# Optimization experiments

Hardware: AMD Instinct MI355X
Metric: run time of the kernel (lower is better)

Reference implementation:

```python
import jax, jax.numpy as jnp
import numpy as np

EPS = 1e-5
ALPHA = 32.0


def setup_inputs() -> dict:
    key = jax.random.key(0)
    k1, k2 = jax.random.split(key)
    M, D, K = 131072, 256, 512
    x = jax.random.normal(k1, (M, D), dtype=jnp.float32)
    ln_weight = jnp.ones((D,), dtype=jnp.float32)
    ln_bias = jnp.zeros((D,), dtype=jnp.float32)
    cluster_center = jax.random.uniform(k2, (K, D), dtype=jnp.float32)
    return {"x": x, "ln_weight": ln_weight, "ln_bias": ln_bias,
            "cluster_center": cluster_center}


def reference(x, ln_weight, ln_bias, cluster_center):
    # CustomLayerNorm: (x - mean) / (std + eps) * w + b  (std unbiased=False,
    # NOTE eps is added to std, not variance, matching the torch module)
    mean = x.mean(axis=-1, keepdims=True)
    std = jnp.sqrt(((x - mean) ** 2).mean(axis=-1, keepdims=True))
    xn = (x - mean) / (std + EPS) * ln_weight + ln_bias

    # Euclidean cdist via sum-of-squares + GEMM, then sqrt (as in source)
    x_sq = (xn * xn).sum(axis=-1, keepdims=True)            # (M, 1)
    c_sq = (cluster_center * cluster_center).sum(axis=-1)   # (K,)
    d2 = x_sq + c_sq[None, :] - 2.0 * (xn @ cluster_center.T)
    x_distance = jnp.sqrt(d2)                               # (M, K)

    # NegSoftAssign: exp(-alpha * d / mean_d), normalized over last dim
    d_mean = x_distance.mean(axis=-1, keepdims=True)
    logits = -ALPHA * (x_distance / d_mean)
    x_distance_assign = jax.nn.softmax(logits, axis=-1)     # (M, K)

    x_rec = x_distance_assign @ cluster_center              # (M, D)
    return (x_distance, x_distance_assign, x_rec)
```

## Files before the change

kernel.cpp:

```cpp
#include <hip/hip_runtime.h>
#include <hip/hip_bf16.h>
#include <cstdint>

#define M_ROWS 131072
#define D_DIM  256
#define K_CL   512

typedef __attribute__((ext_vector_type(4))) float  f4;
typedef __attribute__((ext_vector_type(8))) short  bfrag;
typedef __attribute__((ext_vector_type(4))) float  ffrag;

#define MFMA16(A,B,C) __builtin_amdgcn_mfma_f32_16x16x32_bf16((A),(B),(C),0,0,0)

__device__ __forceinline__ unsigned short f2bf(float f) {
    unsigned int u = __float_as_uint(f);
    u += 0x7FFFu + ((u >> 16) & 1u);
    return (unsigned short)(u >> 16);
}
__device__ __forceinline__ float bf2f(unsigned short u) {
    return __uint_as_float(((unsigned int)u) << 16);
}

__global__ void prep_kernel(const float* __restrict__ C,
                            unsigned short* __restrict__ Cb,
                            unsigned short* __restrict__ Ct,
                            float* __restrict__ csq)
{
    __shared__ unsigned short lds[64 * 264];
    const int tid = threadIdx.x;
    const int kb  = blockIdx.x * 64;
    const int r   = tid >> 2;
    const int q   = tid & 3;

    const float* cr = C + (size_t)(kb + r) * D_DIM;
    float s = 0.f;
    #pragma unroll
    for (int i = 0; i < 16; ++i) {
        const int j = q * 16 + i;
        f4 v = *(const f4*)(cr + j * 4);
        unsigned short u0 = f2bf(v[0]), u1 = f2bf(v[1]), u2 = f2bf(v[2]), u3 = f2bf(v[3]);
        *(ushort4*)(Cb + (size_t)(kb + r) * D_DIM + j * 4) = make_ushort4(u0, u1, u2, u3);
        *(ushort4*)(lds + r * 264 + j * 4)                  = make_ushort4(u0, u1, u2, u3);
        float f0 = bf2f(u0), f1 = bf2f(u1), f2_ = bf2f(u2), f3 = bf2f(u3);
        s += f0 * f0 + f1 * f1 + f2_ * f2_ + f3 * f3;
    }
    s += __shfl_xor(s, 1, 64);
    s += __shfl_xor(s, 2, 64);
    if (q == 0) csq[kb + r] = s;
    __syncthreads();

    #pragma unroll
    for (int c = 0; c < 16; ++c) {
        ushort4 p = make_ushort4(lds[(c * 4 + 0) * 264 + tid],
                                 lds[(c * 4 + 1) * 264 + tid],
                                 lds[(c * 4 + 2) * 264 + tid],
                                 lds[(c * 4 + 3) * 264 + tid]);
        *(ushort4*)(Ct + (size_t)tid * K_CL + kb + c * 4) = p;
    }
}

__global__ __launch_bounds__(256)
void fused_kernel(const float* __restrict__ x,
                  const float* __restrict__ lnw,
                  const float* __restrict__ lnb,
                  const unsigned short* __restrict__ Cb,
                  const unsigned short* __restrict__ Ct,
                  const float* __restrict__ csq,
                  float* __restrict__ out0,
                  float* __restrict__ out1,
                  float* __restrict__ out2)
{
    __shared__ __align__(16) char smem[51712];
    unsigned short* xn_s = (unsigned short*)smem;
    unsigned short* as_s = (unsigned short*)(smem + 16896);
    float* csq_s = (float*)(smem + 16896);
    float* red_a = (float*)(smem + 50176);
    float* red_b = (float*)(smem + 50688);
    float* xsq_s = (float*)(smem + 51200);
    float* sc_s  = (float*)(smem + 51328);
    float* mn_s  = (float*)(smem + 51456);
    float* rn_s  = (float*)(smem + 51584);

    const int tid = threadIdx.x;
    const int w   = tid >> 6;
    const int l   = tid & 63;
    const int g   = l >> 4;
    const int cl  = l & 15;
    const int m0  = blockIdx.x * 32;

    csq_s[tid]       = csq[tid];
    csq_s[tid + 256] = csq[tid + 256];

    {
        const int row = tid >> 3, sub = tid & 7;
        const float* xr = x + (size_t)(m0 + row) * D_DIM;
        f4 xv[8];
        float sum = 0.f, ss = 0.f;
        #pragma unroll
        for (int i = 0; i < 8; ++i) {
            xv[i] = *(const f4*)(xr + (i * 8 + sub) * 4);
            #pragma unroll
            for (int c = 0; c < 4; ++c) { float v = xv[i][c]; sum += v; ss += v * v; }
        }
        #pragma unroll
        for (int msk = 1; msk < 8; msk <<= 1) {
            sum += __shfl_xor(sum, msk, 64);
            ss  += __shfl_xor(ss,  msk, 64);
        }
        const float mean = sum * (1.0f / 256.0f);
        float var = ss * (1.0f / 256.0f) - mean * mean;
        var = fmaxf(var, 0.0f);
        const float inv = 1.0f / (sqrtf(var) + 1e-5f);

        float xsq = 0.f;
        #pragma unroll
        for (int i = 0; i < 8; ++i) {
            f4 wv = *(const f4*)(lnw + (i * 8 + sub) * 4);
            f4 bv = *(const f4*)(lnb + (i * 8 + sub) * 4);
            unsigned short u0, u1, u2, u3;
            {
                float a0 = (xv[i][0] - mean) * inv * wv[0] + bv[0];
                float a1 = (xv[i][1] - mean) * inv * wv[1] + bv[1];
                float a2 = (xv[i][2] - mean) * inv * wv[2] + bv[2];
                float a3 = (xv[i][3] - mean) * inv * wv[3] + bv[3];
                u0 = f2bf(a0); u1 = f2bf(a1); u2 = f2bf(a2); u3 = f2bf(a3);
                float b0 = bf2f(u0), b1 = bf2f(u1), b2 = bf2f(u2), b3 = bf2f(u3);
                xsq += b0 * b0 + b1 * b1 + b2 * b2 + b3 * b3;
            }
            *(ushort4*)(xn_s + row * 264 + (i * 8 + sub) * 4) = make_ushort4(u0, u1, u2, u3);
        }
        #pragma unroll
        for (int msk = 1; msk < 8; msk <<= 1) xsq += __shfl_xor(xsq, msk, 64);
        if (sub == 0) xsq_s[row] = xsq;
    }
    __syncthreads();

    const int nb = w * 128;
    ffrag acc[2][8];
    #pragma unroll
    for (int rt = 0; rt < 2; ++rt)
        #pragma unroll
        for (int nt = 0; nt < 8; ++nt)
            acc[rt][nt] = (ffrag){0.f, 0.f, 0.f, 0.f};
    {
        bfrag a[2][8];
        #pragma unroll
        for (int rt = 0; rt < 2; ++rt)
            #pragma unroll
            for (int ks = 0; ks < 8; ++ks)
                a[rt][ks] = *(const bfrag*)(xn_s + (rt * 16 + cl) * 264 + ks * 32 + g * 8);
        #pragma unroll
        for (int nt = 0; nt < 8; ++nt) {
            const unsigned short* bp = Cb + (size_t)(nb + nt * 16 + cl) * D_DIM + g * 8;
            #pragma unroll
            for (int ks = 0; ks < 8; ++ks) {
                bfrag b = *(const bfrag*)(bp + ks * 32);
                acc[0][nt] = MFMA16(a[0][ks], b, acc[0][nt]);
                acc[1][nt] = MFMA16(a[1][ks], b, acc[1][nt]);
            }
        }
    }

    float xsq_r[2][4];
    #pragma unroll
    for (int rt = 0; rt < 2; ++rt)
        #pragma unroll
        for (int r = 0; r < 4; ++r)
            xsq_r[rt][r] = xsq_s[rt * 16 + g * 4 + r];

    #pragma unroll
    for (int nt = 0; nt < 8; ++nt) {
        const float cs = csq_s[nb + nt * 16 + cl];
        #pragma unroll
        for (int rt = 0; rt < 2; ++rt)
            #pragma unroll
            for (int r = 0; r < 4; ++r) {
                float d2 = xsq_r[rt][r] + cs - 2.0f * acc[rt][nt][r];
                float d  = sqrtf(fmaxf(d2, 0.0f));
                acc[rt][nt][r] = d;
                out0[(size_t)(m0 + rt * 16 + g * 4 + r) * K_CL + nb + nt * 16 + cl] = d;
            }
    }

    {
        float s[2][4], mn[2][4];
        #pragma unroll
        for (int rt = 0; rt < 2; ++rt)
            #pragma unroll
            for (int r = 0; r < 4; ++r) { s[rt][r] = acc[rt][0][r]; mn[rt][r] = acc[rt][0][r]; }
        #pragma unroll
        for (int nt = 1; nt < 8; ++nt)
            #pragma unroll
            for (int rt = 0; rt < 2; ++rt)
                #pragma unroll
                for (int r = 0; r < 4; ++r) {
                    s[rt][r]  += acc[rt][nt][r];
                    mn[rt][r]  = fminf(mn[rt][r], acc[rt][nt][r]);
                }
        #pragma unroll
        for (int msk = 1; msk < 16; msk <<= 1)
            #pragma unroll
            for (int rt = 0; rt < 2; ++rt)
                #pragma unroll
                for (int r = 0; r < 4; ++r) {
                    s[rt][r]  += __shfl_xor(s[rt][r],  msk, 64);
                    mn[rt][r]  = fminf(mn[rt][r], __shfl_xor(mn[rt][r], msk, 64));
                }
        if (cl == 0) {
            #pragma unroll
            for (int rt = 0; rt < 2; ++rt)
                #pragma unroll
                for (int r = 0; r < 4; ++r) {
                    red_a[w * 32 + rt * 16 + g * 4 + r] = s[rt][r];
                    red_b[w * 32 + rt * 16 + g * 4 + r] = mn[rt][r];
                }
        }
    }
    __syncthreads();
    if (tid < 32) {
        float t0 = red_a[tid] + red_a[32 + tid] + red_a[64 + tid] + red_a[96 + tid];
        float mv = fminf(fminf(red_b[tid], red_b[32 + tid]),
                         fminf(red_b[64 + tid], red_b[96 + tid]));
        sc_s[tid] = 16384.0f / t0;
        mn_s[tid] = mv;
    }
    __syncthreads();

    {
        float sc_r[2][4], mnr[2][4], es[2][4];
        #pragma unroll
        for (int rt = 0; rt < 2; ++rt)
            #pragma unroll
            for (int r = 0; r < 4; ++r) {
                sc_r[rt][r] = sc_s[rt * 16 + g * 4 + r];
                mnr[rt][r]  = mn_s[rt * 16 + g * 4 + r];
                es[rt][r]   = 0.f;
            }
        #pragma unroll
        for (int nt = 0; nt < 8; ++nt)
            #pragma unroll
            for (int rt = 0; rt < 2; ++rt)
                #pragma unroll
                for (int r = 0; r < 4; ++r) {
                    float p = __expf((mnr[rt][r] - acc[rt][nt][r]) * sc_r[rt][r]);
                    acc[rt][nt][r] = p;
                    es[rt][r] += p;
                }
        #pragma unroll
        for (int msk = 1; msk < 16; msk <<= 1)
            #pragma unroll
            for (int rt = 0; rt < 2; ++rt)
                #pragma unroll
                for (int r = 0; r < 4; ++r)
                    es[rt][r] += __shfl_xor(es[rt][r], msk, 64);
        if (cl == 0) {
            #pragma unroll
            for (int rt = 0; rt < 2; ++rt)
                #pragma unroll
                for (int r = 0; r < 4; ++r)
                    red_a[w * 32 + rt * 16 + g * 4 + r] = es[rt][r];
        }
    }
    __syncthreads();
    if (tid < 32)
        rn_s[tid] = 1.0f / (red_a[tid] + red_a[32 + tid] + red_a[64 + tid] + red_a[96 + tid]);
    __syncthreads();

    {
        float rn_r[2][4];
        #pragma unroll
        for (int rt = 0; rt < 2; ++rt)
            #pragma unroll
            for (int r = 0; r < 4; ++r)
                rn_r[rt][r] = rn_s[rt * 16 + g * 4 + r];
        #pragma unroll
        for (int nt = 0; nt < 8; ++nt)
            #pragma unroll
            for (int rt = 0; rt < 2; ++rt)
                #pragma unroll
                for (int r = 0; r < 4; ++r) {
                    float av = acc[rt][nt][r] * rn_r[rt][r];
                    out1[(size_t)(m0 + rt * 16 + g * 4 + r) * K_CL + nb + nt * 16 + cl] = av;
                    as_s[(rt * 16 + g * 4 + r) * 520 + nb + nt * 16 + cl] = f2bf(av);
                }
    }
    __syncthreads();

    {
        ffrag acc2[2][4];
        #pragma unroll
        for (int rt = 0; rt < 2; ++rt)
            #pragma unroll
            for (int nt = 0; nt < 4; ++nt)
                acc2[rt][nt] = (ffrag){0.f, 0.f, 0.f, 0.f};
        const int db = w * 64;
        #pragma unroll
        for (int kt = 0; kt < 16; ++kt) {
            bfrag a0 = *(const bfrag*)(as_s + (cl)      * 520 + kt * 32 + g * 8);
            bfrag a1 = *(const bfrag*)(as_s + (16 + cl) * 520 + kt * 32 + g * 8);
            #pragma unroll
            for (int nt = 0; nt < 4; ++nt) {
                bfrag b = *(const bfrag*)(Ct + (size_t)(db + nt * 16 + cl) * K_CL + kt * 32 + g * 8);
                acc2[0][nt] = MFMA16(a0, b, acc2[0][nt]);
                acc2[1][nt] = MFMA16(a1, b, acc2[1][nt]);
            }
        }
        #pragma unroll
        for (int rt = 0; rt < 2; ++rt)
            #pragma unroll
            for (int nt = 0; nt < 4; ++nt)
                #pragma unroll
                for (int r = 0; r < 4; ++r)
                    out2[(size_t)(m0 + rt * 16 + g * 4 + r) * D_DIM + db + nt * 16 + cl]
                        = acc2[rt][nt][r];
    }
}

extern "C" void kernel_launch(void* const* d_in, const int* in_sizes, int n_in,
                              void* d_out, int out_size, void* d_ws, size_t ws_size,
                              hipStream_t stream)
{
    const float* x   = (const float*)d_in[0];
    const float* lnw = (const float*)d_in[1];
    const float* lnb = (const float*)d_in[2];
    const float* C   = (const float*)d_in[3];

    float* out0 = (float*)d_out;
    float* out1 = out0 + (size_t)M_ROWS * K_CL;
    float* out2 = out1 + (size_t)M_ROWS * K_CL;

    unsigned short* Cb = (unsigned short*)d_ws;
    unsigned short* Ct = Cb + (size_t)K_CL * D_DIM;
    float*          cs = (float*)((char*)d_ws + 2u * K_CL * D_DIM * 2u);

    prep_kernel<<<8, 256, 0, stream>>>(C, Cb, Ct, cs);
    fused_kernel<<<M_ROWS / 32, 256, 0, stream>>>(x, lnw, lnb, Cb, Ct, cs,
                                                  out0, out1, out2);
}
```

Before: 330.8 us.

## Halve rows per block to 16 and alias LDS buffers for higher occupancy

Each block now processes 16 rows instead of 32, so each wave holds one 16-row MFMA tile and about half as many accumulator registers. The LDS layout is shrunk by aliasing the assignment buffer onto the normalized-x buffer. Launch bounds now request 4 blocks per CU. The intent is to raise occupancy and hide memory latency. In exchange, every cluster-center B fragment loaded from global memory now feeds half as many MFMAs, which doubles B traffic per row, and twice as many blocks are launched.

Result: slower. 544.7 us (+64.7%).

```diff
diff --git a/kernel.cpp b/kernel.cpp
--- a/kernel.cpp
+++ b/kernel.cpp
@@ -5,6 +5,7 @@
 #define M_ROWS 131072
 #define D_DIM  256
 #define K_CL   512
+#define ROWS_B 16
 
 typedef __attribute__((ext_vector_type(4))) float  f4;
 typedef __attribute__((ext_vector_type(8))) short  bfrag;
@@ -59,7 +60,7 @@
     }
 }
 
-__global__ __launch_bounds__(256)
+__global__ __launch_bounds__(256, 4)
 void fused_kernel(const float* __restrict__ x,
                   const float* __restrict__ lnw,
                   const float* __restrict__ lnb,
@@ -70,40 +71,41 @@
                   float* __restrict__ out1,
                   float* __restrict__ out2)
 {
-    __shared__ __align__(16) char smem[51712];
+    __shared__ __align__(16) char smem[19456];
     unsigned short* xn_s = (unsigned short*)smem;
-    unsigned short* as_s = (unsigned short*)(smem + 16896);
-    float* csq_s = (float*)(smem + 16896);
-    float* red_a = (float*)(smem + 50176);
-    float* red_b = (float*)(smem + 50688);
-    float* xsq_s = (float*)(smem + 51200);
-    float* sc_s  = (float*)(smem + 51328);
-    float* mn_s  = (float*)(smem + 51456);
-    float* rn_s  = (float*)(smem + 51584);
+    unsigned short* as_s = (unsigned short*)smem;
+    float* csq_s = (float*)(smem + 16640);
+    float* red_a = (float*)(smem + 18688);
+    float* red_b = (float*)(smem + 18944);
+    float* xsq_s = (float*)(smem + 19200);
+    float* sc_s  = (float*)(smem + 19264);
+    float* mn_s  = (float*)(smem + 19328);
+    float* rn_s  = (float*)(smem + 19392);
 
     const int tid = threadIdx.x;
     const int w   = tid >> 6;
     const int l   = tid & 63;
     const int g   = l >> 4;
     const int cl  = l & 15;
-    const int m0  = blockIdx.x * 32;
+    const int m0  = blockIdx.x * ROWS_B;
+    const int row = g * 4;
 
     csq_s[tid]       = csq[tid];
     csq_s[tid + 256] = csq[tid + 256];
 
     {
-        const int row = tid >> 3, sub = tid & 7;
-        const float* xr = x + (size_t)(m0 + row) * D_DIM;
-        f4 xv[8];
+        const int rr  = tid >> 4, sub = tid & 15;
+        const float* xr = x + (size_t)(m0 + rr) * D_DIM;
+        f4 xv[4];
         float sum = 0.f, ss = 0.f;
         #pragma unroll
-        for (int i = 0; i < 8; ++i) {
-            xv[i] = *(const f4*)(xr + (i * 8 + sub) * 4);
+        for (int i = 0; i < 4; ++i) {
+            xv[i] = *(const f4*)(xr + (i * 16 + sub) * 4);
             #pragma unroll
             for (int c = 0; c < 4; ++c) { float v = xv[i][c]; sum += v; ss += v * v; }
         }
         #pragma unroll
-        for (int msk = 1; msk < 8; msk <<= 1) {
+        for (int msk = 1; msk < 16; msk <<= 1) {
             sum += __shfl_xor(sum, msk, 64);
             ss  += __shfl_xor(ss,  msk, 64);
         }
@@ -114,205 +116,162 @@
 
         float xsq = 0.f;
         #pragma unroll
-        for (int i = 0; i < 8; ++i) {
-            f4 wv = *(const f4*)(lnw + (i * 8 + sub) * 4);
-            f4 bv = *(const f4*)(lnb + (i * 8 + sub) * 4);
-            unsigned short u0, u1, u2, u3;
-            {
-                float a0 = (xv[i][0] - mean) * inv * wv[0] + bv[0];
-                float a1 = (xv[i][1] - mean) * inv * wv[1] + bv[1];
-                float a2 = (xv[i][2] - mean) * inv * wv[2] + bv[2];
-                float a3 = (xv[i][3] - mean) * inv * wv[3] + bv[3];
-                u0 = f2bf(a0); u1 = f2bf(a1); u2 = f2bf(a2); u3 = f2bf(a3);
-                float b0 = bf2f(u0), b1 = bf2f(u1), b2 = bf2f(u2), b3 = bf2f(u3);
-                xsq += b0 * b0 + b1 * b1 + b2 * b2 + b3 * b3;
-            }
-            *(ushort4*)(xn_s + row * 264 + (i * 8 + sub) * 4) = make_ushort4(u0, u1, u2, u3);
-        }
-        #pragma unroll
-        for (int msk = 1; msk < 8; msk <<= 1) xsq += __shfl_xor(xsq, msk, 64);
-        if (sub == 0) xsq_s[row] = xsq;
+        for (int i = 0; i < 4; ++i) {
+            f4 wv = *(const f4*)(lnw + (i * 16 + sub) * 4);
+            f4 bv = *(const f4*)(lnb + (i * 16 + sub) * 4);
+            float a0 = (xv[i][0] - mean) * inv * wv[0] + bv[0];
+            float a1 = (xv[i][1] - mean) * inv * wv[1] + bv[1];
+            float a2 = (xv[i][2] - mean) * inv * wv[2] + bv[2];
+            float a3 = (xv[i][3] - mean) * inv * wv[3] + bv[3];
+            unsigned short u0 = f2bf(a0), u1 = f2bf(a1), u2 = f2bf(a2), u3 = f2bf(a3);
+            float b0 = bf2f(u0), b1 = bf2f(u1), b2 = bf2f(u2), b3 = bf2f(u3);
+            xsq += b0 * b0 + b1 * b1 + b2 * b2 + b3 * b3;
+            *(ushort4*)(xn_s + rr * 264 + (i * 16 + sub) * 4) = make_ushort4(u0, u1, u2, u3);
+        }
+        #pragma unroll
+        for (int msk = 1; msk < 16; msk <<= 1) xsq += __shfl_xor(xsq, msk, 64);
+        if (sub == 0) xsq_s[rr] = xsq;
     }
     __syncthreads();
 
     const int nb = w * 128;
-    ffrag acc[2][8];
-    #pragma unroll
-    for (int rt = 0; rt < 2; ++rt)
-        #pragma unroll
-        for (int nt = 0; nt < 8; ++nt)
-            acc[rt][nt] = (ffrag){0.f, 0.f, 0.f, 0.f};
-    {
-        bfrag a[2][8];
-        #pragma unroll
-        for (int rt = 0; rt < 2; ++rt)
-            #pragma unroll
-            for (int ks = 0; ks < 8; ++ks)
-                a[rt][ks] = *(const bfrag*)(xn_s + (rt * 16 + cl) * 264 + ks * 32 + g * 8);
+    ffrag acc[8];
+    #pragma unroll
+    for (int nt = 0; nt < 8; ++nt) acc[nt] = (ffrag){0.f, 0.f, 0.f, 0.f};
+    {
+        bfrag a[8];
+        #pragma unroll
+        for (int ks = 0; ks < 8; ++ks)
+            a[ks] = *(const bfrag*)(xn_s + cl * 264 + ks * 32 + g * 8);
         #pragma unroll
         for (int nt = 0; nt < 8; ++nt) {
             const unsigned short* bp = Cb + (size_t)(nb + nt * 16 + cl) * D_DIM + g * 8;
             #pragma unroll
             for (int ks = 0; ks < 8; ++ks) {
                 bfrag b = *(const bfrag*)(bp + ks * 32);
-                acc[0][nt] = MFMA16(a[0][ks], b, acc[0][nt]);
-                acc[1][nt] = MFMA16(a[1][ks], b, acc[1][nt]);
-            }
-        }
-    }
-
-    float xsq_r[2][4];
-    #pragma unroll
-    for (int rt = 0; rt < 2; ++rt)
-        #pragma unroll
-        for (int r = 0; r < 4; ++r)
-            xsq_r[rt][r] = xsq_s[rt * 16 + g * 4 + r];
+                acc[nt] = MFMA16(a[ks], b, acc[nt]);
+            }
+        }
+    }
+
+    float xsq_r[4];
+    #pragma unroll
+    for (int r = 0; r < 4; ++r) xsq_r[r] = xsq_s[row + r];
 
     #pragma unroll
     for (int nt = 0; nt < 8; ++nt) {
         const float cs = csq_s[nb + nt * 16 + cl];
         #pragma unroll
-        for (int rt = 0; rt < 2; ++rt)
-            #pragma unroll
-            for (int r = 0; r < 4; ++r) {
-                float d2 = xsq_r[rt][r] + cs - 2.0f * acc[rt][nt][r];
-                float d  = sqrtf(fmaxf(d2, 0.0f));
-                acc[rt][nt][r] = d;
-                out0[(size_t)(m0 + rt * 16 + g * 4 + r) * K_CL + nb + nt * 16 + cl] = d;
-            }
-    }
-
-    {
-        float s[2][4], mn[2][4];
-        #pragma unroll
-        for (int rt = 0; rt < 2; ++rt)
-            #pragma unroll
-            for (int r = 0; r < 4; ++r) { s[rt][r] = acc[rt][0][r]; mn[rt][r] = acc[rt][0][r]; }
+        for (int r = 0; r < 4; ++r) {
+            float d2 = xsq_r[r] + cs - 2.0f * acc[nt][r];
+            float d  = sqrtf(fmaxf(d2, 0.0f));
+            acc[nt][r] = d;
+            out0[(size_t)(m0 + row + r) * K_CL + nb + nt * 16 + cl] = d;
+        }
+    }
+
+    {
+        float s[4], mn[4];
+        #pragma unroll
+        for (int r = 0; r < 4; ++r) { s[r] = acc[0][r]; mn[r] = acc[0][r]; }
         #pragma unroll
         for (int nt = 1; nt < 8; ++nt)
             #pragma unroll
-            for (int rt = 0; rt < 2; ++rt)
-                #pragma unroll
-                for (int r = 0; r < 4; ++r) {
-                    s[rt][r]  += acc[rt][nt][r];
-                    mn[rt][r]  = fminf(mn[rt][r], acc[rt][nt][r]);
-                }
+            for (int r = 0; r < 4; ++r) {
+                s[r]  += acc[nt][r];
+                mn[r]  = fminf(mn[r], acc[nt][r]);
+            }
         #pragma unroll
         for (int msk = 1; msk < 16; msk <<= 1)
             #pragma unroll
-            for (int rt = 0; rt < 2; ++rt)
-                #pragma unroll
-                for (int r = 0; r < 4; ++r) {
-                    s[rt][r]  += __shfl_xor(s[rt][r],  msk, 64);
-                    mn[rt][r]  = fminf(mn[rt][r], __shfl_xor(mn[rt][r], msk, 64));
-                }
+            for (int r = 0; r < 4; ++r) {
+                s[r]  += __shfl_xor(s[r],  msk, 64);
+                mn[r]  = fminf(mn[r], __shfl_xor(mn[r], msk, 64));
+            }
         if (cl == 0) {
             #pragma unroll
-            for (int rt = 0; rt < 2; ++rt)
-                #pragma unroll
-                for (int r = 0; r < 4; ++r) {
-                    red_a[w * 32 + rt * 16 + g * 4 + r] = s[rt][r];
-                    red_b[w * 32 + rt * 16 + g * 4 + r] = mn[rt][r];
-                }
-        }
-    }
-    __syncthreads();
-    if (tid < 32) {
-        float t0 = red_a[tid] + red_a[32 + tid] + red_a[64 + tid] + red_a[96 + tid];
-        float mv = fminf(fminf(red_b[tid], red_b[32 + tid]),
-                         fminf(red_b[64 + tid], red_b[96 + tid]));
+            for (int r = 0; r < 4; ++r) {
+                red_a[w * 16 + row + r] = s[r];
+                red_b[w * 16 + row + r] = mn[r];
+            }
+        }
+    }
+    __syncthreads();
+    if (tid < 16) {
+        float t0 = red_a[tid] + red_a[16 + tid] + red_a[32 + tid] + red_a[48 + tid];
+        float mv = fminf(fminf(red_b[tid], red_b[16 + tid]),
+                         fminf(red_b[32 + tid], red_b[48 + tid]));
         sc_s[tid] = 16384.0f / t0;
         mn_s[tid] = mv;
     }
     __syncthreads();
 
     {
-        float sc_r[2][4], mnr[2][4], es[2][4];
-        #pragma unroll
-        for (int rt = 0; rt < 2; ++rt)
-            #pragma unroll
-            for (int r = 0; r < 4; ++r) {
-                sc_r[rt][r] = sc_s[rt * 16 + g * 4 + r];
-                mnr[rt][r]  = mn_s[rt * 16 + g * 4 + r];
-                es[rt][r]   = 0.f;
-            }
+        float sc_r[4], mnr[4], es[4];
+        #pragma unroll
+        for (int r = 0; r < 4; ++r) {
+            sc_r[r] = sc_s[row + r];
+            mnr[r]  = mn_s[row + r];
+            es[r]   = 0.f;
+        }
         #pragma unroll
         for (int nt = 0; nt < 8; ++nt)
             #pragma unroll
-            for (int rt = 0; rt < 2; ++rt)
-                #pragma unroll
-                for (int r = 0; r < 4; ++r) {
-                    float p = __expf((mnr[rt][r] - acc[rt][nt][r]) * sc_r[rt][r]);
-                    acc[rt][nt][r] = p;
-                    es[rt][r] += p;
-                }
+            for (int r = 0; r < 4; ++r) {
+                float p = __expf((mnr[r] - acc[nt][r]) * sc_r[r]);
+                acc[nt][r] = p;
+                es[r] += p;
+            }
         #pragma unroll
         for (int msk = 1; msk < 16; msk <<= 1)
             #pragma unroll
-            for (int rt = 0; rt < 2; ++rt)
-                #pragma unroll
-                for (int r = 0; r < 4; ++r)
-                    es[rt][r] += __shfl_xor(es[rt][r], msk, 64);
+            for (int r = 0; r < 4; ++r)
+                es[r] += __shfl_xor(es[r], msk, 64);
         if (cl == 0) {
             #pragma unroll
-            for (int rt = 0; rt < 2; ++rt)
-                #pragma unroll
-                for (int r = 0; r < 4; ++r)
-                    red_a[w * 32 + rt * 16 + g * 4 + r] = es[rt][r];
-        }
-    }
-    __syncthreads();
-    if (tid < 32)
-        rn_s[tid] = 1.0f / (red_a[tid] + red_a[32 + tid] + red_a[64 + tid] + red_a[96 + tid]);
-    __syncthreads();
-
-    {
-        float rn_r[2][4];
-        #pragma unroll
-        for (int rt = 0; rt < 2; ++rt)
-            #pragma unroll
             for (int r = 0; r < 4; ++r)
-                rn_r[rt][r] = rn_s[rt * 16 + g * 4 + r];
+                red_a[w * 16 + row + r] = es[r];
+        }
+    }
+    __syncthreads();
+    if (tid < 16)
+        rn_s[tid] = 1.0f / (red_a[tid] + red_a[16 + tid] + red_a[32 + tid] + red_a[48 + tid]);
+    __syncthreads();
+
+    {
+        float rn_r[4];
+        #pragma unroll
+        for (int r = 0; r < 4; ++r) rn_r[r] = rn_s[row + r];
         #pragma unroll
         for (int nt = 0; nt < 8; ++nt)
             #pragma unroll
-            for (int rt = 0; rt < 2; ++rt)
-                #pragma unroll
-                for (int r = 0; r < 4; ++r) {
-                    float av = acc[rt][nt][r] * rn_r[rt][r];
-                    out1[(size_t)(m0 + rt * 16 + g * 4 + r) * K_CL + nb + nt * 16 + cl] = av;
-                    as_s[(rt * 16 + g * 4 + r) * 520 + nb + nt * 16 + cl] = f2bf(av);
-                }
-    }
-    __syncthreads();
-
-    {
-        ffrag acc2[2][4];
-        #pragma unroll
-        for (int rt = 0; rt < 2; ++rt)
-            #pragma unroll
-            for (int nt = 0; nt < 4; ++nt)
-                acc2[rt][nt] = (ffrag){0.f, 0.f, 0.f, 0.f};
+            for (int r = 0; r < 4; ++r) {
+                float av = acc[nt][r] * rn_r[r];
+                out1[(size_t)(m0 + row + r) * K_CL + nb + nt * 16 + cl] = av;
+                as_s[(row + r) * 520 + nb + nt * 16 + cl] = f2bf(av);
+            }
+    }
+    __syncthreads();
+
+    {
+        ffrag acc2[4];
+        #pragma unroll
+        for (int nt = 0; nt < 4; ++nt) acc2[nt] = (ffrag){0.f, 0.f, 0.f, 0.f};
         const int db = w * 64;
         #pragma unroll
         for (int kt = 0; kt < 16; ++kt) {
-            bfrag a0 = *(const bfrag*)(as_s + (cl)      * 520 + kt * 32 + g * 8);
-            bfrag a1 = *(const bfrag*)(as_s + (16 + cl) * 520 + kt * 32 + g * 8);
+            bfrag a0 = *(const bfrag*)(as_s + cl * 520 + kt * 32 + g * 8);
             #pragma unroll
             for (int nt = 0; nt < 4; ++nt) {
                 bfrag b = *(const bfrag*)(Ct + (size_t)(db + nt * 16 + cl) * K_CL + kt * 32 + g * 8);
-                acc2[0][nt] = MFMA16(a0, b, acc2[0][nt]);
-                acc2[1][nt] = MFMA16(a1, b, acc2[1][nt]);
-            }
-        }
-        #pragma unroll
-        for (int rt = 0; rt < 2; ++rt)
-            #pragma unroll
-            for (int nt = 0; nt < 4; ++nt)
-                #pragma unroll
-                for (int r = 0; r < 4; ++r)
-                    out2[(size_t)(m0 + rt * 16 + g * 4 + r) * D_DIM + db + nt * 16 + cl]
-                        = acc2[rt][nt][r];
+                acc2[nt] = MFMA16(a0, b, acc2[nt]);
+            }
+        }
+        #pragma unroll
+        for (int nt = 0; nt < 4; ++nt)
+            #pragma unroll
+            for (int r = 0; r < 4; ++r)
+                out2[(size_t)(m0 + row + r) * D_DIM + db + nt * 16 + cl] = acc2[nt][r];
     }
 }
 
@@ -334,6 +293,6 @@
     float*          cs = (float*)((char*)d_ws + 2u * K_CL * D_DIM * 2u);
 
     prep_kernel<<<8, 256, 0, stream>>>(C, Cb, Ct, cs);
-    fused_kernel<<<M_ROWS / 32, 256, 0, stream>>>(x, lnw, lnb, Cb, Ct, cs,
-                                                  out0, out1, out2);
-}
+    fused_kernel<<<M_ROWS / ROWS_B, 256, 0, stream>>>(x, lnw, lnb, Cb, Ct, cs,
+                                                      out0, out1, out2);
+}
```

## Double-buffer B-fragment loads for both GEMMs and trim softmax reduction syncs

Applied to the files above, without the earlier changes.

Global loads of cluster-center fragments for both MFMA GEMMs now go through two register buffers, so the next tile's loads are in flight while the current tile's MFMAs run. The first B tiles are issued before the LayerNorm phase to hide their latency. The softmax row-min reduction is dropped, and each thread now combines the per-wave partial sums itself, removing two block barriers and their shared-memory round trips. The cost is higher register pressure, which may lower occupancy. Without the max (min-distance) subtraction, exp can underflow for rows where every distance is much larger than the mean.

After: 410.3 us. +24.0%, slower.

```diff
diff --git a/kernel.cpp b/kernel.cpp
--- a/kernel.cpp
+++ b/kernel.cpp
@@ -5,6 +5,7 @@
 #define M_ROWS 131072
 #define D_DIM  256
 #define K_CL   512
+#define ROWS_B 32
 
 typedef __attribute__((ext_vector_type(4))) float  f4;
 typedef __attribute__((ext_vector_type(8))) short  bfrag;
@@ -70,30 +71,62 @@
                   float* __restrict__ out1,
                   float* __restrict__ out2)
 {
-    __shared__ __align__(16) char smem[51712];
+    __shared__ __align__(16) char smem[51328];
     unsigned short* xn_s = (unsigned short*)smem;
     unsigned short* as_s = (unsigned short*)(smem + 16896);
     float* csq_s = (float*)(smem + 16896);
     float* red_a = (float*)(smem + 50176);
     float* red_b = (float*)(smem + 50688);
     float* xsq_s = (float*)(smem + 51200);
-    float* sc_s  = (float*)(smem + 51328);
-    float* mn_s  = (float*)(smem + 51456);
-    float* rn_s  = (float*)(smem + 51584);
 
     const int tid = threadIdx.x;
     const int w   = tid >> 6;
     const int l   = tid & 63;
     const int g   = l >> 4;
     const int cl  = l & 15;
-    const int m0  = blockIdx.x * 32;
+    const int m0  = blockIdx.x * ROWS_B;
+    const int nb  = w * 128;
+    const int db  = w * 64;
+
+#define LOADB1(BUF, NT) {                                                       \
+    const unsigned short* bp_ = Cb + (size_t)(nb + (NT) * 16 + cl) * D_DIM + g * 8; \
+    _Pragma("unroll")                                                           \
+    for (int i_ = 0; i_ < 8; ++i_) (BUF)[i_] = *(const bfrag*)(bp_ + i_ * 32); }
+
+#define MFMA1(BUF, NT) {                                                        \
+    _Pragma("unroll")                                                           \
+    for (int i_ = 0; i_ < 8; ++i_) {                                            \
+        acc[0][NT] = MFMA16(a[0][i_], (BUF)[i_], acc[0][NT]);                   \
+        acc[1][NT] = MFMA16(a[1][i_], (BUF)[i_], acc[1][NT]); } }
+
+#define LOADB2(BUF, Q) {                                                        \
+    const unsigned short* bp_ = Ct + (size_t)(db + ((Q) & 3) * 16 + cl) * K_CL  \
+                                + ((Q) >> 2) * 256 + g * 8;                     \
+    _Pragma("unroll")                                                           \
+    for (int i_ = 0; i_ < 8; ++i_) (BUF)[i_] = *(const bfrag*)(bp_ + i_ * 32); }
+
+#define LOADA2(KH) {                                                            \
+    _Pragma("unroll")                                                           \
+    for (int i_ = 0; i_ < 8; ++i_) {                                            \
+        a2[0][i_] = *(const bfrag*)(as_s + (cl)      * 520 + (KH) * 256 + i_ * 32 + g * 8); \
+        a2[1][i_] = *(const bfrag*)(as_s + (16 + cl) * 520 + (KH) * 256 + i_ * 32 + g * 8); } }
+
+#define MFMA2(BUF, NT) {                                                        \
+    _Pragma("unroll")                                                           \
+    for (int i_ = 0; i_ < 8; ++i_) {                                            \
+        acc2[0][NT] = MFMA16(a2[0][i_], (BUF)[i_], acc2[0][NT]);                \
+        acc2[1][NT] = MFMA16(a2[1][i_], (BUF)[i_], acc2[1][NT]); } }
+
+    bfrag bA[8], bB[8];
+    LOADB1(bA, 0);
+    LOADB1(bB, 1);
 
     csq_s[tid]       = csq[tid];
     csq_s[tid + 256] = csq[tid + 256];
 
     {
-        const int row = tid >> 3, sub = tid & 7;
-        const float* xr = x + (size_t)(m0 + row) * D_DIM;
+        const int rr = tid >> 3, sub = tid & 7;
+        const float* xr = x + (size_t)(m0 + rr) * D_DIM;
         f4 xv[8];
         float sum = 0.f, ss = 0.f;
         #pragma unroll
@@ -117,49 +150,43 @@
         for (int i = 0; i < 8; ++i) {
             f4 wv = *(const f4*)(lnw + (i * 8 + sub) * 4);
             f4 bv = *(const f4*)(lnb + (i * 8 + sub) * 4);
-            unsigned short u0, u1, u2, u3;
-            {
-                float a0 = (xv[i][0] - mean) * inv * wv[0] + bv[0];
-                float a1 = (xv[i][1] - mean) * inv * wv[1] + bv[1];
-                float a2 = (xv[i][2] - mean) * inv * wv[2] + bv[2];
-                float a3 = (xv[i][3] - mean) * inv * wv[3] + bv[3];
-                u0 = f2bf(a0); u1 = f2bf(a1); u2 = f2bf(a2); u3 = f2bf(a3);
-                float b0 = bf2f(u0), b1 = bf2f(u1), b2 = bf2f(u2), b3 = bf2f(u3);
-                xsq += b0 * b0 + b1 * b1 + b2 * b2 + b3 * b3;
-            }
-            *(ushort4*)(xn_s + row * 264 + (i * 8 + sub) * 4) = make_ushort4(u0, u1, u2, u3);
+            float a0 = (xv[i][0] - mean) * inv * wv[0] + bv[0];
+            float a1 = (xv[i][1] - mean) * inv * wv[1] + bv[1];
+            float a2_ = (xv[i][2] - mean) * inv * wv[2] + bv[2];
+            float a3 = (xv[i][3] - mean) * inv * wv[3] + bv[3];
+            unsigned short u0 = f2bf(a0), u1 = f2bf(a1), u2 = f2bf(a2_), u3 = f2bf(a3);
+            float b0 = bf2f(u0), b1 = bf2f(u1), b2 = bf2f(u2), b3 = bf2f(u3);
+            xsq += b0 * b0 + b1 * b1 + b2 * b2 + b3 * b3;
+            *(ushort4*)(xn_s + rr * 264 + (i * 8 + sub) * 4) = make_ushort4(u0, u1, u2, u3);
         }
         #pragma unroll
         for (int msk = 1; msk < 8; msk <<= 1) xsq += __shfl_xor(xsq, msk, 64);
-        if (sub == 0) xsq_s[row] = xsq;
-    }
-    __syncthreads();
-
-    const int nb = w * 128;
+        if (sub == 0) xsq_s[rr] = xsq;
+    }
+    __syncthreads();
+
+    bfrag a[2][8];
+    #pragma unroll
+    for (int rt = 0; rt < 2; ++rt)
+        #pragma unroll
+        for (int ks = 0; ks < 8; ++ks)
+            a[rt][ks] = *(const bfrag*)(xn_s + (rt * 16 + cl) * 264 + ks * 32 + g * 8);
+
     ffrag acc[2][8];
     #pragma unroll
     for (int rt = 0; rt < 2; ++rt)
         #pragma unroll
         for (int nt = 0; nt < 8; ++nt)
             acc[rt][nt] = (ffrag){0.f, 0.f, 0.f, 0.f};
-    {
-        bfrag a[2][8];
-        #pragma unroll
-        for (int rt = 0; rt < 2; ++rt)
-            #pragma unroll
-            for (int ks = 0; ks < 8; ++ks)
-                a[rt][ks] = *(const bfrag*)(xn_s + (rt * 16 + cl) * 264 + ks * 32 + g * 8);
-        #pragma unroll
-        for (int nt = 0; nt < 8; ++nt) {
-            const unsigned short* bp = Cb + (size_t)(nb + nt * 16 + cl) * D_DIM + g * 8;
-            #pragma unroll
-            for (int ks = 0; ks < 8; ++ks) {
-                bfrag b = *(const bfrag*)(bp + ks * 32);
-                acc[0][nt] = MFMA16(a[0][ks], b, acc[0][nt]);
-                acc[1][nt] = MFMA16(a[1][ks], b, acc[1][nt]);
-            }
-        }
-    }
+
+    MFMA1(bA, 0); LOADB1(bA, 2);
+    MFMA1(bB, 1); LOADB1(bB, 3);
+    MFMA1(bA, 2); LOADB1(bA, 4);
+    MFMA1(bB, 3); LOADB1(bB, 5);
+    MFMA1(bA, 4); LOADB1(bA, 6);
+    MFMA1(bB, 5); LOADB1(bB, 7);
+    MFMA1(bA, 6);
+    MFMA1(bB, 7);
 
     float xsq_r[2][4];
     #pragma unroll
@@ -182,67 +209,60 @@
             }
     }
 
+    LOADB2(bA, 0);
+    LOADB2(bB, 1);
+
     {
-        float s[2][4], mn[2][4];
-        #pragma unroll
-        for (int rt = 0; rt < 2; ++rt)
-            #pragma unroll
-            for (int r = 0; r < 4; ++r) { s[rt][r] = acc[rt][0][r]; mn[rt][r] = acc[rt][0][r]; }
+        float s[2][4];
+        #pragma unroll
+        for (int rt = 0; rt < 2; ++rt)
+            #pragma unroll
+            for (int r = 0; r < 4; ++r) s[rt][r] = acc[rt][0][r];
         #pragma unroll
         for (int nt = 1; nt < 8; ++nt)
             #pragma unroll
             for (int rt = 0; rt < 2; ++rt)
                 #pragma unroll
+                for (int r = 0; r < 4; ++r) s[rt][r] += acc[rt][nt][r];
+        #pragma unroll
+        for (int msk = 1; msk < 16; msk <<= 1)
+            #pragma unroll
+            for (int rt = 0; rt < 2; ++rt)
+                #pragma unroll
+                for (int r = 0; r < 4; ++r) s[rt][r] += __shfl_xor(s[rt][r], msk, 64);
+        if (cl == 0) {
+            #pragma unroll
+            for (int rt = 0; rt < 2; ++rt)
+                #pragma unroll
+                for (int r = 0; r < 4; ++r)
+                    red_a[w * 32 + rt * 16 + g * 4 + r] = s[rt][r];
+        }
+    }
+    __syncthreads();
+
+    float sc_r[2][4];
+    #pragma unroll
+    for (int rt = 0; rt < 2; ++rt)
+        #pragma unroll
+        for (int r = 0; r < 4; ++r) {
+            const int rowid = rt * 16 + g * 4 + r;
+            float t0 = red_a[rowid] + red_a[32 + rowid] + red_a[64 + rowid] + red_a[96 + rowid];
+            sc_r[rt][r] = 16384.0f / t0;
+        }
+
+    {
+        float es[2][4];
+        #pragma unroll
+        for (int rt = 0; rt < 2; ++rt)
+            #pragma unroll
+            for (int r = 0; r < 4; ++r) es[rt][r] = 0.f;
+        #pragma unroll
+        for (int nt = 0; nt < 8; ++nt)
+            #pragma unroll
+            for (int rt = 0; rt < 2; ++rt)
+                #pragma unroll
                 for (int r = 0; r < 4; ++r) {
-                    s[rt][r]  += acc[rt][nt][r];
-                    mn[rt][r]  = fminf(mn[rt][r], acc[rt][nt][r]);
-                }
-        #pragma unroll
-        for (int msk = 1; msk < 16; msk <<= 1)
-            #pragma unroll
-            for (int rt = 0; rt < 2; ++rt)
-                #pragma unroll
-                for (int r = 0; r < 4; ++r) {
-                    s[rt][r]  += __shfl_xor(s[rt][r],  msk, 64);
-                    mn[rt][r]  = fminf(mn[rt][r], __shfl_xor(mn[rt][r], msk, 64));
-                }
-        if (cl == 0) {
-            #pragma unroll
-            for (int rt = 0; rt < 2; ++rt)
-                #pragma unroll
-                for (int r = 0; r < 4; ++r) {
-                    red_a[w * 32 + rt * 16 + g * 4 + r] = s[rt][r];
-                    red_b[w * 32 + rt * 16 + g * 4 + r] = mn[rt][r];
-                }
-        }
-    }
-    __syncthreads();
-    if (tid < 32) {
-        float t0 = red_a[tid] + red_a[32 + tid] + red_a[64 + tid] + red_a[96 + tid];
-        float mv = fminf(fminf(red_b[tid], red_b[32 + tid]),
-                         fminf(red_b[64 + tid], red_b[96 + tid]));
-        sc_s[tid] = 16384.0f / t0;
-        mn_s[tid] = mv;
-    }
-    __syncthreads();
-
-    {
-        float sc_r[2][4], mnr[2][4], es[2][4];
-        #pragma unroll
-        for (int rt = 0; rt < 2; ++rt)
-            #pragma unroll
-            for (int r = 0; r < 4; ++r) {
-                sc_r[rt][r] = sc_s[rt * 16 + g * 4 + r];
-                mnr[rt][r]  = mn_s[rt * 16 + g * 4 + r];
-                es[rt][r]   = 0.f;
-            }
-        #pragma unroll
-        for (int nt = 0; nt < 8; ++nt)
-            #pragma unroll
-            for (int rt = 0; rt < 2; ++rt)
-                #pragma unroll
-                for (int r = 0; r < 4; ++r) {
-                    float p = __expf((mnr[rt][r] - acc[rt][nt][r]) * sc_r[rt][r]);
+                    float p = __expf(-acc[rt][nt][r] * sc_r[rt][r]);
                     acc[rt][nt][r] = p;
                     es[rt][r] += p;
                 }
@@ -258,32 +278,31 @@
             for (int rt = 0; rt < 2; ++rt)
                 #pragma unroll
                 for (int r = 0; r < 4; ++r)
-                    red_a[w * 32 + rt * 16 + g * 4 + r] = es[rt][r];
-        }
-    }
-    __syncthreads();
-    if (tid < 32)
-        rn_s[tid] = 1.0f / (red_a[tid] + red_a[32 + tid] + red_a[64 + tid] + red_a[96 + tid]);
-    __syncthreads();
-
-    {
-        float rn_r[2][4];
-        #pragma unroll
-        for (int rt = 0; rt < 2; ++rt)
-            #pragma unroll
-            for (int r = 0; r < 4; ++r)
-                rn_r[rt][r] = rn_s[rt * 16 + g * 4 + r];
-        #pragma unroll
-        for (int nt = 0; nt < 8; ++nt)
-            #pragma unroll
-            for (int rt = 0; rt < 2; ++rt)
-                #pragma unroll
-                for (int r = 0; r < 4; ++r) {
-                    float av = acc[rt][nt][r] * rn_r[rt][r];
-                    out1[(size_t)(m0 + rt * 16 + g * 4 + r) * K_CL + nb + nt * 16 + cl] = av;
-                    as_s[(rt * 16 + g * 4 + r) * 520 + nb + nt * 16 + cl] = f2bf(av);
-                }
-    }
+                    red_b[w * 32 + rt * 16 + g * 4 + r] = es[rt][r];
+        }
+    }
+    __syncthreads();
+
+    float rn_r[2][4];
+    #pragma unroll
+    for (int rt = 0; rt < 2; ++rt)
+        #pragma unroll
+        for (int r = 0; r < 4; ++r) {
+            const int rowid = rt * 16 + g * 4 + r;
+            rn_r[rt][r] = 1.0f /
+                (red_b[rowid] + red_b[32 + rowid] + red_b[64 + rowid] + red_b[96 + rowid]);
+        }
+
+    #pragma unroll
+    for (int nt = 0; nt < 8; ++nt)
+        #pragma unroll
+        for (int rt = 0; rt < 2; ++rt)
+            #pragma unroll
+            for (int r = 0; r < 4; ++r) {
+                float av = acc[rt][nt][r] * rn_r[rt][r];
+                out1[(size_t)(m0 + rt * 16 + g * 4 + r) * K_CL + nb + nt * 16 + cl] = av;
+                as_s[(rt * 16 + g * 4 + r) * 520 + nb + nt * 16 + cl] = f2bf(av);
+            }
     __syncthreads();
 
     {
@@ -293,18 +312,19 @@
             #pragma unroll
             for (int nt = 0; nt < 4; ++nt)
                 acc2[rt][nt] = (ffrag){0.f, 0.f, 0.f, 0.f};
-        const int db = w * 64;
-        #pragma unroll
-        for (int kt = 0; kt < 16; ++kt) {
-            bfrag a0 = *(const bfrag*)(as_s + (cl)      * 520 + kt * 32 + g * 8);
-            bfrag a1 = *(const bfrag*)(as_s + (16 + cl) * 520 + kt * 32 + g * 8);
-            #pragma unroll
-            for (int nt = 0; nt < 4; ++nt) {
-                bfrag b = *(const bfrag*)(Ct + (size_t)(db + nt * 16 + cl) * K_CL + kt * 32 + g * 8);
-                acc2[0][nt] = MFMA16(a0, b, acc2[0][nt]);
-                acc2[1][nt] = MFMA16(a1, b, acc2[1][nt]);
-            }
-        }
+
+        bfrag a2[2][8];
+        LOADA2(0);
+        MFMA2(bA, 0); LOADB2(bA, 2);
+        MFMA2(bB, 1); LOADB2(bB, 3);
+        MFMA2(bA, 2); LOADB2(bA, 4);
+        MFMA2(bB, 3); LOADB2(bB, 5);
+        LOADA2(1);
+        MFMA2(bA, 0); LOADB2(bA, 6);
+        MFMA2(bB, 1); LOADB2(bB, 7);
+        MFMA2(bA, 2);
+        MFMA2(bB, 3);
+
         #pragma unroll
         for (int rt = 0; rt < 2; ++rt)
             #pragma unroll
@@ -314,6 +334,12 @@
                     out2[(size_t)(m0 + rt * 16 + g * 4 + r) * D_DIM + db + nt * 16 + cl]
                         = acc2[rt][nt][r];
     }
+
+#undef LOADB1
+#undef MFMA1
+#undef LOADB2
+#undef LOADA2
+#undef MFMA2
 }
 
 extern "C" void kernel_launch(void* const* d_in, const int* in_sizes, int n_in,
@@ -334,6 +360,6 @@
     float*          cs = (float*)((char*)d_ws + 2u * K_CL * D_DIM * 2u);
 
     prep_kernel<<<8, 256, 0, stream>>>(C, Cb, Ct, cs);
-    fused_kernel<<<M_ROWS / 32, 256, 0, stream>>>(x, lnw, lnb, Cb, Ct, cs,
-                                                  out0, out1, out2);
-}
+    fused_kernel<<<M_ROWS / ROWS_B, 256, 0, stream>>>(x, lnw, lnb, Cb, Ct, cs,
+                                                      out0, out1, out2);
+}
```
